# Kernel optimization log

Hardware: AMD Instinct MI355X
Metric: run time of the kernel (lower is better)

## Reference

```python
import jax, jax.numpy as jnp
import numpy as np

N_NODES = 100000
IN_F = 256
OUT_F = 128
N_EDGES = 1600000


def setup_inputs() -> dict:
    key = jax.random.key(0)
    k1, k2, k3, k4 = jax.random.split(key, 4)
    inputs = jax.random.normal(k1, (N_NODES, IN_F), dtype=jnp.float32)
    edge = jax.random.randint(k2, (2, N_EDGES), 0, N_NODES, dtype=jnp.int64)
    # xavier_uniform for weight [in, out]
    bw = float(np.sqrt(6.0 / (IN_F + OUT_F)))
    weight = jax.random.uniform(k3, (IN_F, OUT_F), minval=-bw, maxval=bw, dtype=jnp.float32)
    ba = float(np.sqrt(6.0 / (OUT_F + 1)))
    a = jax.random.uniform(k4, (OUT_F, 1), minval=-ba, maxval=ba, dtype=jnp.float32)
    return {"inputs": inputs, "edge": edge, "weight": weight, "a": a}


def reference(inputs, edge, weight, a):
    # h: [N, out_features]
    h = inputs @ weight
    # edge-wise gather + abs-diff: [E, out_features]
    diff = jnp.abs(h[edge[0]] - h[edge[1]])
    # dot with attention vector a, relu, squeeze -> [E]
    edge_weight = jax.nn.relu((diff @ a).squeeze(-1))
    return (h, edge_weight)
```

## Files before the change

kernel.cpp:

```cpp
#include <hip/hip_runtime.h>
#include <hip/hip_bf16.h>
#include <stdint.h>

typedef __bf16 bf16x8 __attribute__((ext_vector_type(8)));
typedef float  f32x4  __attribute__((ext_vector_type(4)));

#define M_NODES 100000
#define K_IN    256
#define N_OUT   128
#define N_EDGE  1600000
#define BM      64
#define BK      64

__global__ __launch_bounds__(256) void gemm_h_valu(
    const float* __restrict__ in,
    const float* __restrict__ w,
    float* __restrict__ h,
    __hip_bfloat16* __restrict__ hmir)
{
    __shared__ float As[BM][BK + 4];
    __shared__ float Ws[BK][N_OUT];

    const int tx = threadIdx.x;
    const int cg = tx & 15;
    const int rg = tx >> 4;
    const int c0 = cg * 8;
    const int row_base = blockIdx.x * BM;

    float acc[4][8];
    #pragma unroll
    for (int i = 0; i < 4; ++i)
        #pragma unroll
        for (int j = 0; j < 8; ++j) acc[i][j] = 0.f;

    for (int kb = 0; kb < K_IN; kb += BK) {
        __syncthreads();
        {
            const int kq = (tx & 15) * 4;
            const int r0 = tx >> 4;
            #pragma unroll
            for (int i = 0; i < 4; ++i) {
                const int row = r0 + 16 * i;
                f32x4 v = {0.f, 0.f, 0.f, 0.f};
                if (row_base + row < M_NODES)
                    v = *(const f32x4*)(in + (size_t)(row_base + row) * K_IN + kb + kq);
                *(f32x4*)&As[row][kq] = v;
            }
        }
        {
            const int cq = (tx & 31) * 4;
            const int k0 = tx >> 5;
            #pragma unroll
            for (int i = 0; i < 8; ++i) {
                const int k = k0 + 8 * i;
                *(f32x4*)&Ws[k][cq] = *(const f32x4*)(w + (size_t)(kb + k) * N_OUT + cq);
            }
        }
        __syncthreads();

        #pragma unroll 8
        for (int k = 0; k < BK; ++k) {
            float wv[8];
            *(f32x4*)&wv[0] = *(const f32x4*)&Ws[k][c0];
            *(f32x4*)&wv[4] = *(const f32x4*)&Ws[k][c0 + 4];
            float av[4];
            #pragma unroll
            for (int i = 0; i < 4; ++i) av[i] = As[rg * 4 + i][k];
            #pragma unroll
            for (int i = 0; i < 4; ++i)
                #pragma unroll
                for (int j = 0; j < 8; ++j)
                    acc[i][j] = fmaf(av[i], wv[j], acc[i][j]);
        }
    }

    #pragma unroll
    for (int i = 0; i < 4; ++i) {
        const int row = row_base + rg * 4 + i;
        if (row >= M_NODES) continue;
        const f32x4 v0 = {acc[i][0], acc[i][1], acc[i][2], acc[i][3]};
        const f32x4 v1 = {acc[i][4], acc[i][5], acc[i][6], acc[i][7]};
        *(f32x4*)(h + (size_t)row * N_OUT + c0)     = v0;
        *(f32x4*)(h + (size_t)row * N_OUT + c0 + 4) = v1;
        if (hmir) {
            bf16x8 o;
            #pragma unroll
            for (int j = 0; j < 8; ++j) o[j] = (__bf16)acc[i][j];
            *(bf16x8*)((__bf16*)hmir + (size_t)row * N_OUT + c0) = o;
        }
    }
}

__device__ inline int detect_i64(const uint32_t* p) {
    return __popcll(__ballot(p[2 * (threadIdx.x & 63) + 1] == 0u)) >= 60;
}

__global__ __launch_bounds__(256) void edge_kernel_bf16(
    const __hip_bfloat16* __restrict__ hm,
    const uint32_t* __restrict__ edge_raw,
    const float* __restrict__ a,
    float* __restrict__ ew,
    int E)
{
    const int e64 = detect_i64(edge_raw);
    const int s = threadIdx.x & 15;
    const int e = (int)((blockIdx.x * 256 + threadIdx.x) >> 4);
    if (e >= E) return;

    int src, dst;
    if (e64) {
        src = (int)edge_raw[2 * (size_t)e];
        dst = (int)edge_raw[2 * ((size_t)E + e)];
    } else {
        const int* e32 = (const int*)edge_raw;
        src = e32[e];
        dst = e32[(size_t)E + e];
    }

    const __bf16* hb = (const __bf16*)hm;
    const bf16x8 hs = *(const bf16x8*)(hb + (size_t)src * N_OUT + s * 8);
    const bf16x8 hd = *(const bf16x8*)(hb + (size_t)dst * N_OUT + s * 8);
    const f32x4 a0 = *(const f32x4*)(a + s * 8);
    const f32x4 a1 = *(const f32x4*)(a + s * 8 + 4);

    float sum = 0.f;
    #pragma unroll
    for (int i = 0; i < 4; ++i)
        sum += fabsf((float)hs[i] - (float)hd[i]) * a0[i];
    #pragma unroll
    for (int i = 0; i < 4; ++i)
        sum += fabsf((float)hs[4 + i] - (float)hd[4 + i]) * a1[i];

    sum += __shfl_xor(sum, 1, 64);
    sum += __shfl_xor(sum, 2, 64);
    sum += __shfl_xor(sum, 4, 64);
    sum += __shfl_xor(sum, 8, 64);

    if (s == 0) ew[e] = fmaxf(sum, 0.f);
}

__global__ __launch_bounds__(256) void edge_kernel_f32(
    const float* __restrict__ h,
    const uint32_t* __restrict__ edge_raw,
    const float* __restrict__ a,
    float* __restrict__ ew,
    int E)
{
    const int e64 = detect_i64(edge_raw);
    const int s = threadIdx.x & 15;
    const int e = (int)((blockIdx.x * 256 + threadIdx.x) >> 4);
    if (e >= E) return;

    int src, dst;
    if (e64) {
        src = (int)edge_raw[2 * (size_t)e];
        dst = (int)edge_raw[2 * ((size_t)E + e)];
    } else {
        const int* e32 = (const int*)edge_raw;
        src = e32[e];
        dst = e32[(size_t)E + e];
    }

    const f32x4 s0 = *(const f32x4*)(h + (size_t)src * N_OUT + s * 8);
    const f32x4 s1 = *(const f32x4*)(h + (size_t)src * N_OUT + s * 8 + 4);
    const f32x4 d0 = *(const f32x4*)(h + (size_t)dst * N_OUT + s * 8);
    const f32x4 d1 = *(const f32x4*)(h + (size_t)dst * N_OUT + s * 8 + 4);
    const f32x4 a0 = *(const f32x4*)(a + s * 8);
    const f32x4 a1 = *(const f32x4*)(a + s * 8 + 4);

    float sum = 0.f;
    #pragma unroll
    for (int i = 0; i < 4; ++i) sum += fabsf(s0[i] - d0[i]) * a0[i];
    #pragma unroll
    for (int i = 0; i < 4; ++i) sum += fabsf(s1[i] - d1[i]) * a1[i];

    sum += __shfl_xor(sum, 1, 64);
    sum += __shfl_xor(sum, 2, 64);
    sum += __shfl_xor(sum, 4, 64);
    sum += __shfl_xor(sum, 8, 64);

    if (s == 0) ew[e] = fmaxf(sum, 0.f);
}

extern "C" void kernel_launch(void* const* d_in, const int* in_sizes, int n_in,
                              void* d_out, int out_size, void* d_ws, size_t ws_size,
                              hipStream_t stream) {
    const float*    in   = (const float*)d_in[0];
    const uint32_t* edge = (const uint32_t*)d_in[1];
    const float*    w    = (const float*)d_in[2];
    const float*    a    = (const float*)d_in[3];

    float* h  = (float*)d_out;
    float* ew = h + (size_t)M_NODES * N_OUT;

    const size_t mirror_bytes = (size_t)M_NODES * N_OUT * sizeof(__hip_bfloat16);
    __hip_bfloat16* hmir =
        (ws_size >= mirror_bytes) ? (__hip_bfloat16*)d_ws : nullptr;

    gemm_h_valu<<<dim3((M_NODES + BM - 1) / BM), dim3(256), 0, stream>>>(
        in, w, h, hmir);

    const int eblocks = (N_EDGE * 16 + 255) / 256;
    if (hmir)
        edge_kernel_bf16<<<dim3(eblocks), dim3(256), 0, stream>>>(
            hmir, edge, a, ew, N_EDGE);
    else
        edge_kernel_f32<<<dim3(eblocks), dim3(256), 0, stream>>>(
            h, edge, a, ew, N_EDGE);
}
```

Measured before the change: 346.7 us.

## Replace FP32 VALU node GEMM with bf16 MFMA kernel reading operands directly

The shared-memory FP32 FMA GEMM that computes h is replaced by a kernel using 16x16x32 bf16 MFMA instructions. Each wave loads A rows and W columns straight from global memory, converting them to bf16 in registers, with no LDS staging. Output is written with nontemporal scalar stores plus a bf16 mirror for the edge kernel. The aim is to cut the GEMM's ALU cost. In exchange, inputs are rounded to bf16, so h loses precision. W reads are strided and uncoalesced, output stores are narrower, and the fallback path writes the mirror into a possibly undersized workspace.

```diff
diff --git a/kernel.cpp b/kernel.cpp
--- a/kernel.cpp
+++ b/kernel.cpp
@@ -9,84 +9,80 @@
 #define K_IN    256
 #define N_OUT   128
 #define N_EDGE  1600000
-#define BM      64
-#define BK      64
-
-__global__ __launch_bounds__(256) void gemm_h_valu(
+
+__global__ __launch_bounds__(256) void gemm_h_mfma(
     const float* __restrict__ in,
     const float* __restrict__ w,
     float* __restrict__ h,
     __hip_bfloat16* __restrict__ hmir)
 {
-    __shared__ float As[BM][BK + 4];
-    __shared__ float Ws[BK][N_OUT];
-
-    const int tx = threadIdx.x;
-    const int cg = tx & 15;
-    const int rg = tx >> 4;
-    const int c0 = cg * 8;
-    const int row_base = blockIdx.x * BM;
-
-    float acc[4][8];
-    #pragma unroll
-    for (int i = 0; i < 4; ++i)
-        #pragma unroll
-        for (int j = 0; j < 8; ++j) acc[i][j] = 0.f;
-
-    for (int kb = 0; kb < K_IN; kb += BK) {
-        __syncthreads();
-        {
-            const int kq = (tx & 15) * 4;
-            const int r0 = tx >> 4;
-            #pragma unroll
-            for (int i = 0; i < 4; ++i) {
-                const int row = r0 + 16 * i;
-                f32x4 v = {0.f, 0.f, 0.f, 0.f};
-                if (row_base + row < M_NODES)
-                    v = *(const f32x4*)(in + (size_t)(row_base + row) * K_IN + kb + kq);
-                *(f32x4*)&As[row][kq] = v;
+    const int lane = threadIdx.x & 63;
+    const int wave = threadIdx.x >> 6;
+    const int m0   = blockIdx.x * 64;
+    const int nb   = wave * 32;
+
+    const int lr = lane & 15;
+    const int q  = lane >> 4;
+
+    f32x4 acc[4][2];
+    #pragma unroll
+    for (int mt = 0; mt < 4; ++mt)
+        #pragma unroll
+        for (int nt = 0; nt < 2; ++nt)
+            acc[mt][nt] = f32x4{0.f, 0.f, 0.f, 0.f};
+
+    for (int kk = 0; kk < K_IN; kk += 32) {
+        const int ka = kk + q * 8;
+
+        bf16x8 afrag[4];
+        #pragma unroll
+        for (int mt = 0; mt < 4; ++mt) {
+            const int row = m0 + mt * 16 + lr;
+            if (row < M_NODES) {
+                const float* ap = in + (size_t)row * K_IN + ka;
+                const f32x4 a0 = *(const f32x4*)ap;
+                const f32x4 a1 = *(const f32x4*)(ap + 4);
+                #pragma unroll
+                for (int j = 0; j < 4; ++j) {
+                    afrag[mt][j]     = (__bf16)a0[j];
+                    afrag[mt][4 + j] = (__bf16)a1[j];
+                }
+            } else {
+                #pragma unroll
+                for (int j = 0; j < 8; ++j) afrag[mt][j] = (__bf16)0.f;
             }
         }
-        {
-            const int cq = (tx & 31) * 4;
-            const int k0 = tx >> 5;
+
+        bf16x8 bfrag[2];
+        #pragma unroll
+        for (int nt = 0; nt < 2; ++nt) {
+            const int col = nb + nt * 16 + lr;
             #pragma unroll
-            for (int i = 0; i < 8; ++i) {
-                const int k = k0 + 8 * i;
-                *(f32x4*)&Ws[k][cq] = *(const f32x4*)(w + (size_t)(kb + k) * N_OUT + cq);
+            for (int j = 0; j < 8; ++j)
+                bfrag[nt][j] = (__bf16)w[(size_t)(ka + j) * N_OUT + col];
+        }
+
+        #pragma unroll
+        for (int mt = 0; mt < 4; ++mt)
+            #pragma unroll
+            for (int nt = 0; nt < 2; ++nt)
+                acc[mt][nt] = __builtin_amdgcn_mfma_f32_16x16x32_bf16(
+                    afrag[mt], bfrag[nt], acc[mt][nt], 0, 0, 0);
+    }
+
+    #pragma unroll
+    for (int mt = 0; mt < 4; ++mt) {
+        const int rb = m0 + mt * 16 + q * 4;
+        if (rb >= M_NODES) continue;
+        #pragma unroll
+        for (int nt = 0; nt < 2; ++nt) {
+            const int col = nb + nt * 16 + lr;
+            #pragma unroll
+            for (int r = 0; r < 4; ++r) {
+                const float v = acc[mt][nt][r];
+                __builtin_nontemporal_store(v, h + (size_t)(rb + r) * N_OUT + col);
+                hmir[(size_t)(rb + r) * N_OUT + col] = __float2bfloat16(v);
             }
-        }
-        __syncthreads();
-
-        #pragma unroll 8
-        for (int k = 0; k < BK; ++k) {
-            float wv[8];
-            *(f32x4*)&wv[0] = *(const f32x4*)&Ws[k][c0];
-            *(f32x4*)&wv[4] = *(const f32x4*)&Ws[k][c0 + 4];
-            float av[4];
-            #pragma unroll
-            for (int i = 0; i < 4; ++i) av[i] = As[rg * 4 + i][k];
-            #pragma unroll
-            for (int i = 0; i < 4; ++i)
-                #pragma unroll
-                for (int j = 0; j < 8; ++j)
-                    acc[i][j] = fmaf(av[i], wv[j], acc[i][j]);
-        }
-    }
-
-    #pragma unroll
-    for (int i = 0; i < 4; ++i) {
-        const int row = row_base + rg * 4 + i;
-        if (row >= M_NODES) continue;
-        const f32x4 v0 = {acc[i][0], acc[i][1], acc[i][2], acc[i][3]};
-        const f32x4 v1 = {acc[i][4], acc[i][5], acc[i][6], acc[i][7]};
-        *(f32x4*)(h + (size_t)row * N_OUT + c0)     = v0;
-        *(f32x4*)(h + (size_t)row * N_OUT + c0 + 4) = v1;
-        if (hmir) {
-            bf16x8 o;
-            #pragma unroll
-            for (int j = 0; j < 8; ++j) o[j] = (__bf16)acc[i][j];
-            *(bf16x8*)((__bf16*)hmir + (size_t)row * N_OUT + c0) = o;
         }
     }
 }
@@ -197,14 +193,17 @@
     __hip_bfloat16* hmir =
         (ws_size >= mirror_bytes) ? (__hip_bfloat16*)d_ws : nullptr;
 
-    gemm_h_valu<<<dim3((M_NODES + BM - 1) / BM), dim3(256), 0, stream>>>(
-        in, w, h, hmir);
-
-    const int eblocks = (N_EDGE * 16 + 255) / 256;
-    if (hmir)
+    if (hmir) {
+        gemm_h_mfma<<<dim3((M_NODES + 63) / 64), dim3(256), 0, stream>>>(
+            in, w, h, hmir);
+        const int eblocks = (N_EDGE * 16 + 255) / 256;
         edge_kernel_bf16<<<dim3(eblocks), dim3(256), 0, stream>>>(
             hmir, edge, a, ew, N_EDGE);
-    else
+    } else {
+        gemm_h_mfma<<<dim3((M_NODES + 63) / 64), dim3(256), 0, stream>>>(
+            in, w, h, (__hip_bfloat16*)d_ws);
+        const int eblocks = (N_EDGE * 16 + 255) / 256;
         edge_kernel_f32<<<dim3(eblocks), dim3(256), 0, stream>>>(
             h, edge, a, ew, N_EDGE);
-}
+    }
+}
```

Result: faster. 324.4 us (-6.5%).
